# Performance work log

Hardware: AMD Instinct MI355X
Metric: run time of the kernel (lower is better)

The kernel has to match this reference:

```python
import jax, jax.numpy as jnp
import numpy as np

IDIM = 128
C = 3
NB_SAMPLES = 128
R = 32768
SH_C0 = 0.28209479177387814
SH_C1 = 0.4886025119029199
SH_C2 = np.array([1.0925484305920792, -1.0925484305920792, 0.31539156525252005,
                  -1.0925484305920792, 0.5462742152960396], dtype=np.float32)


def eval_sh_bases(d):
    # d: (R,3) unit directions -> (R,9) degree-2 real SH basis
    x, y, z = d[:, 0], d[:, 1], d[:, 2]
    return jnp.stack([
        jnp.full_like(x, SH_C0),
        -SH_C1 * y, SH_C1 * z, -SH_C1 * x,
        SH_C2[0] * x * y, SH_C2[1] * y * z,
        SH_C2[2] * (2.0 * z * z - x * x - y * y),
        SH_C2[3] * x * z, SH_C2[4] * (x * x - y * y)], axis=-1)


def trilerp(pts, grid):
    # pts: (N,3) in voxel coords (box_min=0, delta_voxel=1); grid: (D,D,D,F)
    D = grid.shape[0]
    p = jnp.clip(pts, 0.0, D - 1 - 1e-4)
    i0 = jnp.floor(p).astype(jnp.int32)
    w = p - i0.astype(p.dtype)          # (N,3) fractional weights
    i1 = jnp.minimum(i0 + 1, D - 1)
    out = jnp.zeros((pts.shape[0], grid.shape[-1]), dtype=p.dtype)
    for dx in (0, 1):
        wx = w[:, 0] if dx else 1.0 - w[:, 0]
        ix = i1[:, 0] if dx else i0[:, 0]
        for dy in (0, 1):
            wy = w[:, 1] if dy else 1.0 - w[:, 1]
            iy = i1[:, 1] if dy else i0[:, 1]
            for dz in (0, 1):
                wz = w[:, 2] if dz else 1.0 - w[:, 2]
                iz = i1[:, 2] if dz else i0[:, 2]
                out = out + (wx * wy * wz)[:, None] * grid[ix, iy, iz]
    return out


def setup_inputs() -> dict:
    key = jax.random.key(0)
    k = jax.random.split(key, 6)
    x = jax.random.uniform(k[0], (R, 3), jnp.float32) * (IDIM - 1)
    d = jax.random.normal(k[1], (R, 3), jnp.float32)
    d = d / jnp.linalg.norm(d, axis=1, keepdims=True)
    tmin = jax.random.uniform(k[2], (R,), jnp.float32) * 5.0
    tmax = tmin + 20.0 + jax.random.uniform(k[3], (R,), jnp.float32) * 80.0
    grid = jax.random.uniform(k[4], (IDIM, IDIM, IDIM, 9 * C), jnp.float32)
    opacity = jax.random.uniform(k[5], (IDIM, IDIM, IDIM, 1), jnp.float32)
    return {"x": x, "d": d, "tmin": tmin, "tmax": tmax, "grid": grid, "opacity": opacity}


def reference(x, d, tmin, tmax, grid, opacity):
    nb_rays = x.shape[0]
    # samples = arange(0.05, 0.95, 1/nb_samples): S entries
    S = int(np.floor(0.9 * NB_SAMPLES - 1e-6)) + 1
    base = 0.05 + jnp.arange(S, dtype=x.dtype) / NB_SAMPLES            # (S,)
    samples = (tmax - tmin)[:, None] * base[None, :] + tmin[:, None]   # (R,S)
    pts = x[:, None, :] + samples[..., None] * d[:, None, :]           # (R,S,3)
    sh = eval_sh_bases(d)                                              # (R,9)
    flat = pts.reshape(-1, 3)
    coeffs = trilerp(flat, grid).reshape(nb_rays, S, C, 9)             # (R,S,C,9)
    op = jnp.clip(trilerp(flat, opacity), 0.0, 100000.0).reshape(nb_rays, S)
    harm = coeffs * sh[:, None, None, :]                               # (R,S,C,9)
    samples_color = jnp.clip(harm.sum(axis=3) + 0.5, 0.0, 100000.0)    # (R,S,C)
    deltas = samples[:, 1:] - samples[:, :-1]                          # (R,S-1)
    dts = -(deltas * op[:, :-1])
    cum = jnp.concatenate([jnp.zeros((nb_rays, 1), dtype=x.dtype),
                           jnp.cumsum(dts, axis=1)[:, :-1]], axis=1)
    w = jnp.exp(cum) * (1.0 - jnp.exp(dts))                            # (R,S-1)
    rays_color = jnp.sum(w[..., None] * samples_color[:, :-1, :], axis=1)  # (R,C)
    return rays_color
```

## Files before the change

### kernel.cpp

```cpp
#include <hip/hip_runtime.h>

#define NS 115
#define WEPS 5e-5f
#define LOG_TSKIP -6.9078f

typedef float f32x4 __attribute__((ext_vector_type(4)));
typedef float f32x2 __attribute__((ext_vector_type(2)));

struct SH9 { float a,b,c,d,e,f,g,h,i; };

__device__ __forceinline__ f32x4 load4(const float* p) { f32x4 v; __builtin_memcpy(&v, p, 16); return v; }
__device__ __forceinline__ f32x2 load2(const float* p) { f32x2 v; __builtin_memcpy(&v, p, 8);  return v; }

__device__ __forceinline__ void pos_to_cell(float px, float py, float pz,
                                            int& ibase, float* wxs, float* wys, float* wzs) {
    px = fminf(fmaxf(px, 0.0f), 126.9999f);
    py = fminf(fmaxf(py, 0.0f), 126.9999f);
    pz = fminf(fmaxf(pz, 0.0f), 126.9999f);
    int ix = (int)px, iy = (int)py, iz = (int)pz;
    float wx = px - (float)ix, wy = py - (float)iy, wz = pz - (float)iz;
    ibase = (ix << 14) + (iy << 7) + iz;
    wxs[0] = 1.0f - wx; wxs[1] = wx;
    wys[0] = 1.0f - wy; wys[1] = wy;
    wzs[0] = 1.0f - wz; wzs[1] = wz;
}

__device__ __forceinline__ float eval_op(float px, float py, float pz,
                                         const float* __restrict__ opa) {
    int ibase; float wxs[2], wys[2], wzs[2];
    pos_to_cell(px, py, pz, ibase, wxs, wys, wzs);
    float op = 0.0f;
    #pragma unroll
    for (int cx = 0; cx < 2; ++cx)
    #pragma unroll
    for (int cy = 0; cy < 2; ++cy) {
        int idx = ibase + (cx << 14) + (cy << 7);
        f32x2 pr = load2(opa + idx);
        float wxy = wxs[cx] * wys[cy];
        op = fmaf(wxy * wzs[0], pr.x, op);
        op = fmaf(wxy * wzs[1], pr.y, op);
    }
    return fminf(fmaxf(op, 0.0f), 100000.0f);
}

__device__ __forceinline__ float wave_incl_scan(float v, int lane) {
    #pragma unroll
    for (int off = 1; off < 64; off <<= 1) {
        float n = __shfl_up(v, (unsigned)off, 64);
        if (lane >= off) v += n;
    }
    return v;
}

__device__ __forceinline__ SH9 make_sh(float ddx, float ddy, float ddz) {
    SH9 sh;
    sh.a = 0.28209479177387814f;
    sh.b = -0.4886025119029199f * ddy;
    sh.c =  0.4886025119029199f * ddz;
    sh.d = -0.4886025119029199f * ddx;
    sh.e =  1.0925484305920792f * ddx * ddy;
    sh.f = -1.0925484305920792f * ddy * ddz;
    sh.g =  0.31539156525252005f * (2.0f*ddz*ddz - ddx*ddx - ddy*ddy);
    sh.h = -1.0925484305920792f * ddx * ddz;
    sh.i =  0.5462742152960396f * (ddx*ddx - ddy*ddy);
    return sh;
}

__global__ __launch_bounds__(256) void fused_color_kernel(
    const float* __restrict__ x, const float* __restrict__ d,
    const float* __restrict__ tmin, const float* __restrict__ tmax,
    const float* __restrict__ opa, const float* __restrict__ grid,
    float* __restrict__ out, int nrays)
{
    int gtid = blockIdx.x * blockDim.x + threadIdx.x;
    int ray = __builtin_amdgcn_readfirstlane(gtid >> 6);
    int lane = threadIdx.x & 63;
    if (ray >= nrays) return;
    int qd  = lane >> 2;
    int sub = lane & 3;

    float ox = x[3*ray+0], oy = x[3*ray+1], oz = x[3*ray+2];
    float ddx = d[3*ray+0], ddy = d[3*ray+1], ddz = d[3*ray+2];
    float t0 = tmin[ray];
    float range = tmax[ray] - t0;
    float delta = range * 0.0078125f;
    SH9 sh = make_sh(ddx, ddy, ddz);

    float tt = range * (0.05f + (float)lane * 0.0078125f) + t0;
    float px0 = ox + tt*ddx, py0 = oy + tt*ddy, pz0 = oz + tt*ddz;
    float opv = eval_op(px0, py0, pz0, opa);
    float dts = -delta * opv;
    float incl = wave_incl_scan(dts, lane);
    float cum = incl - dts;
    float total0 = __shfl(incl, 63, 64);
    float w0 = __expf(cum) * (1.0f - __expf(dts));

    float w1 = 0.0f;
    if (total0 > LOG_TSKIP) {
        int s1 = 64 + lane;
        float dts1 = 0.0f;
        if (s1 < NS) {
            float t1s = range * (0.05f + (float)s1 * 0.0078125f) + t0;
            float qx = ox + t1s*ddx, qy = oy + t1s*ddy, qz = oz + t1s*ddz;
            dts1 = -delta * eval_op(qx, qy, qz, opa);
        }
        float incl1 = wave_incl_scan(dts1, lane);
        float cum1 = total0 + incl1 - dts1;
        w1 = __expf(cum1) * (1.0f - __expf(dts1));
    }

    float s00,s01,s02,s03,s04,s05,s06,s07;
    float s10,s11,s12,s13,s14,s15,s16,s17;
    if (sub == 0) {
        s00=sh.a;s01=sh.b;s02=sh.c;s03=sh.d;s04=sh.e;s05=sh.f;s06=sh.g;s07=sh.h;
        s10=0.f;s11=0.f;s12=0.f;s13=0.f;s14=0.f;s15=0.f;s16=0.f;s17=0.f;
    } else if (sub == 1) {
        s00=sh.i;s01=0.f;s02=0.f;s03=0.f;s04=0.f;s05=0.f;s06=0.f;s07=0.f;
        s10=0.f;s11=sh.a;s12=sh.b;s13=sh.c;s14=sh.d;s15=sh.e;s16=sh.f;s17=sh.g;
    } else if (sub == 2) {
        s00=sh.h;s01=sh.i;s02=0.f;s03=0.f;s04=0.f;s05=0.f;s06=0.f;s07=0.f;
        s10=0.f;s11=0.f;s12=sh.a;s13=sh.b;s14=sh.c;s15=sh.d;s16=sh.e;s17=sh.f;
    } else {
        s00=0.f;s01=sh.g;s02=sh.h;s03=sh.i;s04=0.f;s05=0.f;s06=0.f;s07=0.f;
        s10=0.f;s11=0.f;s12=0.f;s13=0.f;s14=0.f;s15=0.f;s16=0.f;s17=0.f;
    }
    int offa = (sub == 3) ? 23 : (sub << 3);
    int offb = (sub == 3) ? 23 : offa + 4;

    unsigned long long b0 = __ballot(w0 > WEPS);
    unsigned long long b1 = __ballot(w1 > WEPS);

    float accR = 0.0f, accG = 0.0f, accB = 0.0f;

    #pragma unroll 1
    for (int p = 0; p < 8; ++p) {
        unsigned long long bsel = (p < 4) ? b0 : b1;
        int shl = (p & 3) << 4;
        if (((bsel >> shl) & 0xFFFFull) == 0) continue;
        int s = (p << 4) + qd;
        float ws = __shfl((p < 4) ? w0 : w1, s & 63, 64);
        if (ws > WEPS) {
            float st = range * (0.05f + (float)s * 0.0078125f) + t0;
            float px = ox + st*ddx, py = oy + st*ddy, pz = oz + st*ddz;
            int ibase; float wxs[2], wys[2], wzs[2];
            pos_to_cell(px, py, pz, ibase, wxs, wys, wzs);
            float d0a = 0.0f, d1a = 0.0f;
            #pragma unroll
            for (int cx = 0; cx < 2; ++cx)
            #pragma unroll
            for (int cy = 0; cy < 2; ++cy)
            #pragma unroll
            for (int cz = 0; cz < 2; ++cz) {
                int idx = ibase + (cx << 14) + (cy << 7) + cz;
                float wc = wxs[cx] * wys[cy] * wzs[cz];
                const float* cp = grid + (size_t)idx * 27;
                f32x4 va = load4(cp + offa);
                f32x4 vb = load4(cp + offb);
                float f0=va.x, f1=va.y, f2=va.z, f3=va.w;
                float f4=vb.x, f5=vb.y, f6=vb.z, f7=vb.w;
                float e0 = s00*f0 + s01*f1 + s02*f2 + s03*f3
                         + s04*f4 + s05*f5 + s06*f6 + s07*f7;
                float e1 = s10*f0 + s11*f1 + s12*f2 + s13*f3
                         + s14*f4 + s15*f5 + s16*f6 + s17*f7;
                d0a = fmaf(wc, e0, d0a);
                d1a = fmaf(wc, e1, d1a);
            }
            float rp = (sub < 2)  ? d0a : 0.0f;
            float gp = (sub == 1) ? d1a : ((sub == 2) ? d0a : 0.0f);
            float bp = (sub == 2) ? d1a : ((sub == 3) ? d0a : 0.0f);
            rp += __shfl_xor(rp, 1, 64); rp += __shfl_xor(rp, 2, 64);
            gp += __shfl_xor(gp, 1, 64); gp += __shfl_xor(gp, 2, 64);
            bp += __shfl_xor(bp, 1, 64); bp += __shfl_xor(bp, 2, 64);
            float cr = fminf(fmaxf(rp + 0.5f, 0.0f), 100000.0f);
            float cg = fminf(fmaxf(gp + 0.5f, 0.0f), 100000.0f);
            float cb = fminf(fmaxf(bp + 0.5f, 0.0f), 100000.0f);
            accR = fmaf(ws, cr, accR);
            accG = fmaf(ws, cg, accG);
            accB = fmaf(ws, cb, accB);
        }
    }

    #pragma unroll
    for (int off = 4; off < 64; off <<= 1) {
        accR += __shfl_xor(accR, off, 64);
        accG += __shfl_xor(accG, off, 64);
        accB += __shfl_xor(accB, off, 64);
    }
    if (lane == 0) {
        out[3*ray+0] = accR;
        out[3*ray+1] = accG;
        out[3*ray+2] = accB;
    }
}

extern "C" void kernel_launch(void* const* d_in, const int* in_sizes, int n_in,
                              void* d_out, int out_size, void* d_ws, size_t ws_size,
                              hipStream_t stream) {
    const float* x    = (const float*)d_in[0];
    const float* d    = (const float*)d_in[1];
    const float* tmin = (const float*)d_in[2];
    const float* tmax = (const float*)d_in[3];
    const float* grid = (const float*)d_in[4];
    const float* opa  = (const float*)d_in[5];
    float* out = (float*)d_out;

    int nrays = in_sizes[0] / 3;
    int blocks = (nrays * 64 + 255) / 256;

    (void)d_ws; (void)ws_size;
    fused_color_kernel<<<blocks, 256, 0, stream>>>(x, d, tmin, tmax, opa, grid, out, nrays);
}
```

Measured before the change: 390.1 us.

## Assign one sample per lane for color evaluation instead of quad-split channels

Color work moves from four lanes cooperating on one sample, each holding a slice of the 27 coefficients, to each lane evaluating all 27 coefficients for its own sample. The cell indices and weights from the opacity pass are reused, and the per-sample quad shuffles and ballot-driven loop are removed. The cost is seven vector loads per corner per lane, which leaves lanes with low weight idle in a divergent pattern and raises register pressure. Memory access also becomes less coalesced, because lanes now touch different cells instead of adjacent pieces of the same cell.

```diff
diff --git a/kernel.cpp b/kernel.cpp
--- a/kernel.cpp
+++ b/kernel.cpp
@@ -25,10 +25,8 @@
     wzs[0] = 1.0f - wz; wzs[1] = wz;
 }
 
-__device__ __forceinline__ float eval_op(float px, float py, float pz,
-                                         const float* __restrict__ opa) {
-    int ibase; float wxs[2], wys[2], wzs[2];
-    pos_to_cell(px, py, pz, ibase, wxs, wys, wzs);
+__device__ __forceinline__ float op_cell(int ibase, const float* wxs, const float* wys,
+                                         const float* wzs, const float* __restrict__ opa) {
     float op = 0.0f;
     #pragma unroll
     for (int cx = 0; cx < 2; ++cx)
@@ -41,6 +39,42 @@
         op = fmaf(wxy * wzs[1], pr.y, op);
     }
     return fminf(fmaxf(op, 0.0f), 100000.0f);
+}
+
+__device__ __forceinline__ void color_cell(int ibase, const float* wxs, const float* wys,
+                                           const float* wzs, const float* __restrict__ grid,
+                                           const SH9& sh,
+                                           float& cr, float& cg, float& cb) {
+    float r = 0.0f, g = 0.0f, b = 0.0f;
+    #pragma unroll
+    for (int cx = 0; cx < 2; ++cx)
+    #pragma unroll
+    for (int cy = 0; cy < 2; ++cy)
+    #pragma unroll
+    for (int cz = 0; cz < 2; ++cz) {
+        int idx = ibase + (cx << 14) + (cy << 7) + cz;
+        float wc = wxs[cx] * wys[cy] * wzs[cz];
+        const float* cp = grid + (size_t)idx * 27;
+        f32x4 v0 = load4(cp);
+        f32x4 v1 = load4(cp + 4);
+        f32x4 v2 = load4(cp + 8);
+        f32x4 v3 = load4(cp + 12);
+        f32x4 v4 = load4(cp + 16);
+        f32x4 v5 = load4(cp + 20);
+        f32x4 v6 = load4(cp + 23);
+        float c0 = sh.a*v0.x + sh.b*v0.y + sh.c*v0.z + sh.d*v0.w
+                 + sh.e*v1.x + sh.f*v1.y + sh.g*v1.z + sh.h*v1.w + sh.i*v2.x;
+        float c1 = sh.a*v2.y + sh.b*v2.z + sh.c*v2.w + sh.d*v3.x
+                 + sh.e*v3.y + sh.f*v3.z + sh.g*v3.w + sh.h*v4.x + sh.i*v4.y;
+        float c2 = sh.a*v4.z + sh.b*v4.w + sh.c*v5.x + sh.d*v5.y
+                 + sh.e*v5.z + sh.f*v5.w + sh.g*v6.y + sh.h*v6.z + sh.i*v6.w;
+        r = fmaf(wc, c0, r);
+        g = fmaf(wc, c1, g);
+        b = fmaf(wc, c2, b);
+    }
+    cr = fminf(fmaxf(r + 0.5f, 0.0f), 100000.0f);
+    cg = fminf(fmaxf(g + 0.5f, 0.0f), 100000.0f);
+    cb = fminf(fmaxf(b + 0.5f, 0.0f), 100000.0f);
 }
 
 __device__ __forceinline__ float wave_incl_scan(float v, int lane) {
@@ -66,7 +100,7 @@
     return sh;
 }
 
-__global__ __launch_bounds__(256) void fused_color_kernel(
+__global__ __launch_bounds__(256) void fused_kernel(
     const float* __restrict__ x, const float* __restrict__ d,
     const float* __restrict__ tmin, const float* __restrict__ tmax,
     const float* __restrict__ opa, const float* __restrict__ grid,
@@ -76,8 +110,6 @@
     int ray = __builtin_amdgcn_readfirstlane(gtid >> 6);
     int lane = threadIdx.x & 63;
     if (ray >= nrays) return;
-    int qd  = lane >> 2;
-    int sub = lane & 3;
 
     float ox = x[3*ray+0], oy = x[3*ray+1], oz = x[3*ray+2];
     float ddx = d[3*ray+0], ddy = d[3*ray+1], ddz = d[3*ray+2];
@@ -86,102 +118,50 @@
     float delta = range * 0.0078125f;
     SH9 sh = make_sh(ddx, ddy, ddz);
 
-    float tt = range * (0.05f + (float)lane * 0.0078125f) + t0;
-    float px0 = ox + tt*ddx, py0 = oy + tt*ddy, pz0 = oz + tt*ddz;
-    float opv = eval_op(px0, py0, pz0, opa);
-    float dts = -delta * opv;
-    float incl = wave_incl_scan(dts, lane);
-    float cum = incl - dts;
-    float total0 = __shfl(incl, 63, 64);
-    float w0 = __expf(cum) * (1.0f - __expf(dts));
-
-    float w1 = 0.0f;
-    if (total0 > LOG_TSKIP) {
-        int s1 = 64 + lane;
-        float dts1 = 0.0f;
-        if (s1 < NS) {
-            float t1s = range * (0.05f + (float)s1 * 0.0078125f) + t0;
-            float qx = ox + t1s*ddx, qy = oy + t1s*ddy, qz = oz + t1s*ddz;
-            dts1 = -delta * eval_op(qx, qy, qz, opa);
-        }
-        float incl1 = wave_incl_scan(dts1, lane);
-        float cum1 = total0 + incl1 - dts1;
-        w1 = __expf(cum1) * (1.0f - __expf(dts1));
-    }
-
-    float s00,s01,s02,s03,s04,s05,s06,s07;
-    float s10,s11,s12,s13,s14,s15,s16,s17;
-    if (sub == 0) {
-        s00=sh.a;s01=sh.b;s02=sh.c;s03=sh.d;s04=sh.e;s05=sh.f;s06=sh.g;s07=sh.h;
-        s10=0.f;s11=0.f;s12=0.f;s13=0.f;s14=0.f;s15=0.f;s16=0.f;s17=0.f;
-    } else if (sub == 1) {
-        s00=sh.i;s01=0.f;s02=0.f;s03=0.f;s04=0.f;s05=0.f;s06=0.f;s07=0.f;
-        s10=0.f;s11=sh.a;s12=sh.b;s13=sh.c;s14=sh.d;s15=sh.e;s16=sh.f;s17=sh.g;
-    } else if (sub == 2) {
-        s00=sh.h;s01=sh.i;s02=0.f;s03=0.f;s04=0.f;s05=0.f;s06=0.f;s07=0.f;
-        s10=0.f;s11=0.f;s12=sh.a;s13=sh.b;s14=sh.c;s15=sh.d;s16=sh.e;s17=sh.f;
-    } else {
-        s00=0.f;s01=sh.g;s02=sh.h;s03=sh.i;s04=0.f;s05=0.f;s06=0.f;s07=0.f;
-        s10=0.f;s11=0.f;s12=0.f;s13=0.f;s14=0.f;s15=0.f;s16=0.f;s17=0.f;
-    }
-    int offa = (sub == 3) ? 23 : (sub << 3);
-    int offb = (sub == 3) ? 23 : offa + 4;
-
-    unsigned long long b0 = __ballot(w0 > WEPS);
-    unsigned long long b1 = __ballot(w1 > WEPS);
-
     float accR = 0.0f, accG = 0.0f, accB = 0.0f;
 
-    #pragma unroll 1
-    for (int p = 0; p < 8; ++p) {
-        unsigned long long bsel = (p < 4) ? b0 : b1;
-        int shl = (p & 3) << 4;
-        if (((bsel >> shl) & 0xFFFFull) == 0) continue;
-        int s = (p << 4) + qd;
-        float ws = __shfl((p < 4) ? w0 : w1, s & 63, 64);
-        if (ws > WEPS) {
-            float st = range * (0.05f + (float)s * 0.0078125f) + t0;
-            float px = ox + st*ddx, py = oy + st*ddy, pz = oz + st*ddz;
-            int ibase; float wxs[2], wys[2], wzs[2];
-            pos_to_cell(px, py, pz, ibase, wxs, wys, wzs);
-            float d0a = 0.0f, d1a = 0.0f;
-            #pragma unroll
-            for (int cx = 0; cx < 2; ++cx)
-            #pragma unroll
-            for (int cy = 0; cy < 2; ++cy)
-            #pragma unroll
-            for (int cz = 0; cz < 2; ++cz) {
-                int idx = ibase + (cx << 14) + (cy << 7) + cz;
-                float wc = wxs[cx] * wys[cy] * wzs[cz];
-                const float* cp = grid + (size_t)idx * 27;
-                f32x4 va = load4(cp + offa);
-                f32x4 vb = load4(cp + offb);
-                float f0=va.x, f1=va.y, f2=va.z, f3=va.w;
-                float f4=vb.x, f5=vb.y, f6=vb.z, f7=vb.w;
-                float e0 = s00*f0 + s01*f1 + s02*f2 + s03*f3
-                         + s04*f4 + s05*f5 + s06*f6 + s07*f7;
-                float e1 = s10*f0 + s11*f1 + s12*f2 + s13*f3
-                         + s14*f4 + s15*f5 + s16*f6 + s17*f7;
-                d0a = fmaf(wc, e0, d0a);
-                d1a = fmaf(wc, e1, d1a);
+    {
+        float tt = range * (0.05f + (float)lane * 0.0078125f) + t0;
+        float px = ox + tt*ddx, py = oy + tt*ddy, pz = oz + tt*ddz;
+        int ib; float wxs[2], wys[2], wzs[2];
+        pos_to_cell(px, py, pz, ib, wxs, wys, wzs);
+        float opv = op_cell(ib, wxs, wys, wzs, opa);
+        float dts = -delta * opv;
+        float incl = wave_incl_scan(dts, lane);
+        float cum = incl - dts;
+        float total0 = __shfl(incl, 63, 64);
+        float w0 = __expf(cum) * (1.0f - __expf(dts));
+        if (w0 > WEPS) {
+            float cr, cg, cb;
+            color_cell(ib, wxs, wys, wzs, grid, sh, cr, cg, cb);
+            accR = w0 * cr; accG = w0 * cg; accB = w0 * cb;
+        }
+
+        if (total0 > LOG_TSKIP) {
+            int s1 = 64 + lane;
+            float dts1 = 0.0f;
+            int ib1 = 0; float wxs1[2] = {0.f,0.f}, wys1[2] = {0.f,0.f}, wzs1[2] = {0.f,0.f};
+            if (s1 < NS) {
+                float t1s = range * (0.05f + (float)s1 * 0.0078125f) + t0;
+                float qx = ox + t1s*ddx, qy = oy + t1s*ddy, qz = oz + t1s*ddz;
+                pos_to_cell(qx, qy, qz, ib1, wxs1, wys1, wzs1);
+                dts1 = -delta * op_cell(ib1, wxs1, wys1, wzs1, opa);
             }
-            float rp = (sub < 2)  ? d0a : 0.0f;
-            float gp = (sub == 1) ? d1a : ((sub == 2) ? d0a : 0.0f);
-            float bp = (sub == 2) ? d1a : ((sub == 3) ? d0a : 0.0f);
-            rp += __shfl_xor(rp, 1, 64); rp += __shfl_xor(rp, 2, 64);
-            gp += __shfl_xor(gp, 1, 64); gp += __shfl_xor(gp, 2, 64);
-            bp += __shfl_xor(bp, 1, 64); bp += __shfl_xor(bp, 2, 64);
-            float cr = fminf(fmaxf(rp + 0.5f, 0.0f), 100000.0f);
-            float cg = fminf(fmaxf(gp + 0.5f, 0.0f), 100000.0f);
-            float cb = fminf(fmaxf(bp + 0.5f, 0.0f), 100000.0f);
-            accR = fmaf(ws, cr, accR);
-            accG = fmaf(ws, cg, accG);
-            accB = fmaf(ws, cb, accB);
+            float incl1 = wave_incl_scan(dts1, lane);
+            float cum1 = total0 + incl1 - dts1;
+            float w1 = __expf(cum1) * (1.0f - __expf(dts1));
+            if (w1 > WEPS) {
+                float cr, cg, cb;
+                color_cell(ib1, wxs1, wys1, wzs1, grid, sh, cr, cg, cb);
+                accR = fmaf(w1, cr, accR);
+                accG = fmaf(w1, cg, accG);
+                accB = fmaf(w1, cb, accB);
+            }
         }
     }
 
     #pragma unroll
-    for (int off = 4; off < 64; off <<= 1) {
+    for (int off = 32; off > 0; off >>= 1) {
         accR += __shfl_xor(accR, off, 64);
         accG += __shfl_xor(accG, off, 64);
         accB += __shfl_xor(accB, off, 64);
@@ -208,5 +188,5 @@
     int blocks = (nrays * 64 + 255) / 256;
 
     (void)d_ws; (void)ws_size;
-    fused_color_kernel<<<blocks, 256, 0, stream>>>(x, d, tmin, tmax, opa, grid, out, nrays);
+    fused_kernel<<<blocks, 256, 0, stream>>>(x, d, tmin, tmax, opa, grid, out, nrays);
 }
```

Measured after the change: 401.7 us. 3.0% more time.
